# Performance work log

Hardware: AMD Instinct MI355X
Metric: run time of the kernel (lower is better)

Reference implementation:

```python
import jax, jax.numpy as jnp
import numpy as np

B, S, T = 32, 64, 64          # batch, src_len, tgt_len
E, H, V = 512, 1024, 32000    # embed, hidden, vocab
WSCALE = 0.05                 # keep tanh/sigmoid in sane range


def setup_inputs() -> dict:
    key = jax.random.key(0)
    ks = jax.random.split(key, 14)
    n = lambda k, shp: jax.random.normal(k, shp, jnp.float32)
    return {
        "target": jax.random.randint(ks[0], (B, T), 0, V),
        "src_enc": n(ks[1], (B, S, 2 * H)),
        "h0": n(ks[2], (B, H)),
        "c0": n(ks[3], (B, H)),
        "emb": n(ks[4], (V, E)) * WSCALE,
        "W_ih": n(ks[5], (E, 4 * H)) * WSCALE,
        "W_hh": n(ks[6], (H, 4 * H)) * WSCALE,
        "b_rnn": jnp.zeros((4 * H,), jnp.float32),
        "W_attn": n(ks[7], (2 * H, H)) * WSCALE,
        "b_attn": jnp.zeros((H,), jnp.float32),
        "W_comb": n(ks[8], (2 * H, H)) * WSCALE,
        "b_comb": jnp.zeros((H,), jnp.float32),
        "W_out": n(ks[9], (H, V)) * WSCALE,
        "b_out": jnp.zeros((V,), jnp.float32),
    }


def reference(target, src_enc, h0, c0, emb, W_ih, W_hh, b_rnn,
              W_attn, b_attn, W_comb, b_comb, W_out, b_out):
    # Pre-project encoder states once (decode() applies attention.linear up front)
    enc_proj = src_enc @ W_attn + b_attn                 # [B,S,H]
    xs = emb[target[:, :-1]]                             # teacher forcing [B,T-1,E]
    xs = jnp.swapaxes(xs, 0, 1)                          # [T-1,B,E] for scan

    def step(carry, x_t):
        h, c = carry
        # LSTM cell (torch gate order i, f, g, o)
        gates = x_t @ W_ih + h @ W_hh + b_rnn            # [B,4H]
        i, f, g, o = jnp.split(gates, 4, axis=-1)
        c = jax.nn.sigmoid(f) * c + jax.nn.sigmoid(i) * jnp.tanh(g)
        h = jax.nn.sigmoid(o) * jnp.tanh(c)
        # Bilinear attention: score = h^T (W_attn e_s) over source positions
        scores = jnp.einsum('bsh,bh->bs', enc_proj, h)
        attn = jax.nn.softmax(scores, axis=-1)
        ctx = jnp.einsum('bs,bsh->bh', attn, enc_proj)   # [B,H]
        out = jnp.tanh(jnp.concatenate([h, ctx], axis=-1) @ W_comb + b_comb)
        return (h, c), out

    _, outs = jax.lax.scan(step, (h0, c0), xs)           # [T-1,B,H]
    outs = jnp.swapaxes(outs, 0, 1)                      # [B,T-1,H]
    logits = outs @ W_out + b_out                        # [B,T-1,V]
    return logits
```

## Files before the change

### kernel.cpp

```cpp
#include <hip/hip_runtime.h>
#include <stdint.h>

#define NB    32
#define NS    64
#define TDEC  63
#define NE    512
#define NH    1024
#define NV    32000

typedef float  floatx4 __attribute__((ext_vector_type(4)));
typedef short  short8  __attribute__((ext_vector_type(8)));
typedef short  short4v __attribute__((ext_vector_type(4)));

__device__ __forceinline__ float bf2f(short s) {
  return __uint_as_float(((uint32_t)(uint16_t)s) << 16);
}
__device__ __forceinline__ short f2bf(float f) {
  uint32_t u = __float_as_uint(f);
  uint32_t r = (u + 0x7fffu + ((u >> 16) & 1u)) >> 16;
  return (short)(uint16_t)r;
}
__device__ __forceinline__ float sigm(float x) { return 1.f / (1.f + expf(-x)); }

template<int PERM>
__global__ __launch_bounds__(256) void transpose_bf(
    const float* __restrict__ W, short* __restrict__ Wt, int K, int N)
{
  __shared__ float tile[32][33];
  int k0 = blockIdx.x * 32, n0 = blockIdx.y * 32;
  int tx = threadIdx.x & 31, ty = threadIdx.x >> 5;
#pragma unroll
  for (int r = 0; r < 32; r += 8)
    tile[ty + r][tx] = W[(size_t)(k0 + ty + r) * N + n0 + tx];
  __syncthreads();
  int kq = threadIdx.x & 7, nl = threadIdx.x >> 3;
  int n = n0 + nl;
  int rr = PERM ? ((n & 1023) * 4 + (n >> 10)) : n;
  short4v v;
#pragma unroll
  for (int q = 0; q < 4; ++q) v[q] = f2bf(tile[kq * 4 + q][nl]);
  *(short4v*)&Wt[(size_t)rr * K + k0 + kq * 4] = v;
}

template<int PERM>
__global__ __launch_bounds__(256) void transpose_bf_split(
    const float* __restrict__ W, short* __restrict__ Wt_hi,
    short* __restrict__ Wt_lo, int K, int N)
{
  __shared__ float tile[32][33];
  int k0 = blockIdx.x * 32, n0 = blockIdx.y * 32;
  int tx = threadIdx.x & 31, ty = threadIdx.x >> 5;
#pragma unroll
  for (int r = 0; r < 32; r += 8)
    tile[ty + r][tx] = W[(size_t)(k0 + ty + r) * N + n0 + tx];
  __syncthreads();
  int kq = threadIdx.x & 7, nl = threadIdx.x >> 3;
  int n = n0 + nl;
  int rr = PERM ? ((n & 1023) * 4 + (n >> 10)) : n;
  short4v vh, vl;
#pragma unroll
  for (int q = 0; q < 4; ++q) {
    float v = tile[kq * 4 + q][nl];
    short h = f2bf(v);
    vh[q] = h;
    vl[q] = f2bf(v - bf2f(h));
  }
  size_t o = (size_t)rr * K + k0 + kq * 4;
  *(short4v*)&Wt_hi[o] = vh;
  *(short4v*)&Wt_lo[o] = vl;
}

__global__ __launch_bounds__(256) void gather_init(
    const int* __restrict__ target, const float* __restrict__ emb,
    const float* __restrict__ h0, const float* __restrict__ c0,
    const float* __restrict__ brnn,
    short* __restrict__ xs, float* __restrict__ hf_all,
    short* __restrict__ hhi_all, short* __restrict__ hlo_all,
    float* __restrict__ c_buf, float* __restrict__ brnn_p)
{
  const int NXS = TDEC * NB * NE;
  const int HN = NH * NB;
  int total = NXS + 2 * HN + 4096;
  for (int idx = blockIdx.x * 256 + threadIdx.x; idx < total; idx += gridDim.x * 256) {
    if (idx < NXS) {
      int row = idx >> 9, e = idx & 511;
      int t = row >> 5, b = row & 31;
      int token = target[b * 64 + t];
      xs[idx] = f2bf(emb[(size_t)token * NE + e]);
    } else if (idx < NXS + HN) {
      int r = idx - NXS;
      float v = h0[r];
      hf_all[r] = v;
      short hh = f2bf(v);
      hhi_all[r] = hh;
      hlo_all[r] = f2bf(v - bf2f(hh));
    } else if (idx < NXS + 2 * HN) {
      int r = idx - NXS - HN;
      c_buf[r] = c0[r];
    } else {
      int c = idx - NXS - 2 * HN;
      brnn_p[c] = brnn[(c & 3) * 1024 + (c >> 2)];
    }
  }
}

template<int OUT_BF>
__global__ __launch_bounds__(256) void gemm_kernel(
    const short* __restrict__ Ab, const short* __restrict__ Bt,
    void* __restrict__ Cptr, const float* __restrict__ bias,
    int M, int N, int K)
{
  __shared__ short As[128 * 40];
  __shared__ short Bs[128 * 40];
  __shared__ float cst[OUT_BF ? 1 : 32 * 132];
  const int m0 = blockIdx.x * 128;
  const int n0 = blockIdx.y * 128;
  const int tid = threadIdx.x;
  const int lane = tid & 63;
  const int wid = tid >> 6;
  const int wr = wid >> 1, wc = wid & 1;

  floatx4 acc[4][4] = {};
  const int row = tid >> 1;
  const int kh  = (tid & 1) << 4;

  for (int k0 = 0; k0 < K; k0 += 32) {
    {
      int gm = m0 + row;
      short8 lo, hi;
      if (gm < M) {
        const short* src = Ab + (size_t)gm * K + k0 + kh;
        lo = *(const short8*)src;
        hi = *(const short8*)(src + 8);
      } else {
#pragma unroll
        for (int c = 0; c < 8; ++c) { lo[c] = 0; hi[c] = 0; }
      }
      *(short8*)&As[row * 40 + kh]     = lo;
      *(short8*)&As[row * 40 + kh + 8] = hi;
    }
    {
      const short* src = Bt + (size_t)(n0 + row) * K + k0 + kh;
      *(short8*)&Bs[row * 40 + kh]     = *(const short8*)src;
      *(short8*)&Bs[row * 40 + kh + 8] = *(const short8*)(src + 8);
    }
    __syncthreads();

    const int kA = (lane >> 4) << 3;
    const int rsel = lane & 15;
    short8 af[4], bfr[4];
#pragma unroll
    for (int mi = 0; mi < 4; ++mi)
      af[mi] = *(const short8*)&As[(wr * 64 + mi * 16 + rsel) * 40 + kA];
#pragma unroll
    for (int ni = 0; ni < 4; ++ni)
      bfr[ni] = *(const short8*)&Bs[(wc * 64 + ni * 16 + rsel) * 40 + kA];
#pragma unroll
    for (int mi = 0; mi < 4; ++mi)
#pragma unroll
      for (int ni = 0; ni < 4; ++ni)
        acc[mi][ni] = __builtin_amdgcn_mfma_f32_16x16x32_bf16(af[mi], bfr[ni], acc[mi][ni], 0, 0, 0);
    __syncthreads();
  }

  const int crow = (lane >> 4) * 4;
  const int ccol = lane & 15;
  if (OUT_BF) {
#pragma unroll
    for (int mi = 0; mi < 4; ++mi) {
#pragma unroll
      for (int ni = 0; ni < 4; ++ni) {
        int gn = n0 + wc * 64 + ni * 16 + ccol;
        float bv = bias[gn];
#pragma unroll
        for (int i = 0; i < 4; ++i) {
          int gm = m0 + wr * 64 + mi * 16 + crow + i;
          if (gm < M)
            ((short*)Cptr)[(size_t)gm * N + gn] = f2bf(acc[mi][ni][i] + bv);
        }
      }
    }
  } else {
#pragma unroll
    for (int p = 0; p < 4; ++p) {
      __syncthreads();
      if (wr == (p >> 1)) {
        int mi0 = (p & 1) * 2;
#pragma unroll
        for (int mm = 0; mm < 2; ++mm) {
#pragma unroll
          for (int ni = 0; ni < 4; ++ni) {
            int c = wc * 64 + ni * 16 + ccol;
#pragma unroll
            for (int i = 0; i < 4; ++i)
              cst[(mm * 16 + crow + i) * 132 + c] = acc[mi0 + mm][ni][i];
          }
        }
      }
      __syncthreads();
#pragma unroll
      for (int rep = 0; rep < 4; ++rep) {
        int cell = tid + rep * 256;
        int r = cell >> 5, q = cell & 31;
        int gm = m0 + p * 32 + r;
        int gn = n0 + q * 4;
        if (gm < M) {
          float4 bv = *(const float4*)&bias[gn];
          float4 v;
          v.x = cst[r * 132 + q * 4 + 0] + bv.x;
          v.y = cst[r * 132 + q * 4 + 1] + bv.y;
          v.z = cst[r * 132 + q * 4 + 2] + bv.z;
          v.w = cst[r * 132 + q * 4 + 3] + bv.w;
          *(float4*)&((float*)Cptr)[(size_t)gm * N + gn] = v;
        }
      }
    }
  }
}

__global__ __launch_bounds__(256) void gemm_split(
    const float* __restrict__ A, const short* __restrict__ Bt_hi,
    const short* __restrict__ Bt_lo, float* __restrict__ C,
    const float* __restrict__ bias, int M, int N, int K)
{
  __shared__ short As_hi[128 * 40];
  __shared__ short As_lo[128 * 40];
  __shared__ short Bs_hi[128 * 40];
  __shared__ short Bs_lo[128 * 40];
  const int m0 = blockIdx.x * 128;
  const int n0 = blockIdx.y * 128;
  const int tid = threadIdx.x;
  const int lane = tid & 63;
  const int wid = tid >> 6;
  const int wr = wid >> 1, wc = wid & 1;

  floatx4 acc[4][4] = {};
  const int row = tid >> 1;
  const int kh  = (tid & 1) << 4;

  for (int k0 = 0; k0 < K; k0 += 32) {
    {
      const float* src = A + (size_t)(m0 + row) * K + k0 + kh;
      short8 h0v, h1, l0, l1;
#pragma unroll
      for (int c = 0; c < 8; ++c) {
        float v = src[c];
        short h = f2bf(v); h0v[c] = h; l0[c] = f2bf(v - bf2f(h));
        float w = src[c + 8];
        short g = f2bf(w); h1[c] = g; l1[c] = f2bf(w - bf2f(g));
      }
      *(short8*)&As_hi[row * 40 + kh]     = h0v;
      *(short8*)&As_hi[row * 40 + kh + 8] = h1;
      *(short8*)&As_lo[row * 40 + kh]     = l0;
      *(short8*)&As_lo[row * 40 + kh + 8] = l1;
    }
    {
      size_t o = (size_t)(n0 + row) * K + k0 + kh;
      *(short8*)&Bs_hi[row * 40 + kh]     = *(const short8*)(Bt_hi + o);
      *(short8*)&Bs_hi[row * 40 + kh + 8] = *(const short8*)(Bt_hi + o + 8);
      *(short8*)&Bs_lo[row * 40 + kh]     = *(const short8*)(Bt_lo + o);
      *(short8*)&Bs_lo[row * 40 + kh + 8] = *(const short8*)(Bt_lo + o + 8);
    }
    __syncthreads();

    const int kA = (lane >> 4) << 3;
    const int rsel = lane & 15;
    short8 ah[4], al[4], bh[4], bl[4];
#pragma unroll
    for (int mi = 0; mi < 4; ++mi) {
      int off = (wr * 64 + mi * 16 + rsel) * 40 + kA;
      ah[mi] = *(const short8*)&As_hi[off];
      al[mi] = *(const short8*)&As_lo[off];
    }
#pragma unroll
    for (int ni = 0; ni < 4; ++ni) {
      int off = (wc * 64 + ni * 16 + rsel) * 40 + kA;
      bh[ni] = *(const short8*)&Bs_hi[off];
      bl[ni] = *(const short8*)&Bs_lo[off];
    }
#pragma unroll
    for (int mi = 0; mi < 4; ++mi)
#pragma unroll
      for (int ni = 0; ni < 4; ++ni) {
        floatx4 a = acc[mi][ni];
        a = __builtin_amdgcn_mfma_f32_16x16x32_bf16(al[mi], bh[ni], a, 0, 0, 0);
        a = __builtin_amdgcn_mfma_f32_16x16x32_bf16(ah[mi], bl[ni], a, 0, 0, 0);
        a = __builtin_amdgcn_mfma_f32_16x16x32_bf16(ah[mi], bh[ni], a, 0, 0, 0);
        acc[mi][ni] = a;
      }
    __syncthreads();
  }

  const int crow = (lane >> 4) * 4;
  const int ccol = lane & 15;
#pragma unroll
  for (int mi = 0; mi < 4; ++mi) {
#pragma unroll
    for (int ni = 0; ni < 4; ++ni) {
      int gn = n0 + wc * 64 + ni * 16 + ccol;
      float bv = bias[gn];
#pragma unroll
      for (int i = 0; i < 4; ++i) {
        int gm = m0 + wr * 64 + mi * 16 + crow + i;
        C[(size_t)gm * N + gn] = acc[mi][ni][i] + bv;
      }
    }
  }
}

__global__ __launch_bounds__(512) void scan_a(
    int t,
    const short* __restrict__ Whp_hi,
    const short* __restrict__ Whp_lo,
    const short* __restrict__ gatesx,
    short* __restrict__ hhi_all,
    short* __restrict__ hlo_all,
    float* __restrict__ hf_all,
    float* __restrict__ c_buf)
{
  __shared__ float smem[8 * 32 * 33];
  const int blk = blockIdx.x;
  const int tid = threadIdx.x;
  const int lane = tid & 63;
  const int wid = tid >> 6;
  const int rsel = lane & 15;
  const int kA = (lane >> 4) * 8;
  const int crow = (lane >> 4) * 4;
  const int ccol = lane & 15;

  const size_t spv = (size_t)t * (NH * NB);
  const size_t snw = (size_t)(t + 1) * (NH * NB);
  const short* Hh = hhi_all + spv;
  const short* Hl = hlo_all + spv;
  const int c0 = blk * 32;
  const int kb = wid * 128;

  floatx4 acc[2][2] = {};
  const short* wh0 = Whp_hi + (size_t)(c0 + rsel) * NH + kb + kA;
  const short* wl0 = Whp_lo + (size_t)(c0 + rsel) * NH + kb + kA;
  const short* wh1 = Whp_hi + (size_t)(c0 + 16 + rsel) * NH + kb + kA;
  const short* wl1 = Whp_lo + (size_t)(c0 + 16 + rsel) * NH + kb + kA;
  const short* ha0 = Hh + (size_t)rsel * NH + kb + kA;
  const short* la0 = Hl + (size_t)rsel * NH + kb + kA;
  const short* ha1 = Hh + (size_t)(16 + rsel) * NH + kb + kA;
  const short* la1 = Hl + (size_t)(16 + rsel) * NH + kb + kA;
#pragma unroll
  for (int kk = 0; kk < 4; ++kk) {
    int k0 = kk * 32;
    short8 a0h = *(const short8*)(ha0 + k0);
    short8 a0l = *(const short8*)(la0 + k0);
    short8 a1h = *(const short8*)(ha1 + k0);
    short8 a1l = *(const short8*)(la1 + k0);
    short8 b0h = *(const short8*)(wh0 + k0);
    short8 b0l = *(const short8*)(wl0 + k0);
    short8 b1h = *(const short8*)(wh1 + k0);
    short8 b1l = *(const short8*)(wl1 + k0);
    acc[0][0] = __builtin_amdgcn_mfma_f32_16x16x32_bf16(a0l, b0h, acc[0][0], 0, 0, 0);
    acc[0][0] = __builtin_amdgcn_mfma_f32_16x16x32_bf16(a0h, b0l, acc[0][0], 0, 0, 0);
    acc[0][0] = __builtin_amdgcn_mfma_f32_16x16x32_bf16(a0h, b0h, acc[0][0], 0, 0, 0);
    acc[0][1] = __builtin_amdgcn_mfma_f32_16x16x32_bf16(a0l, b1h, acc[0][1], 0, 0, 0);
    acc[0][1] = __builtin_amdgcn_mfma_f32_16x16x32_bf16(a0h, b1l, acc[0][1], 0, 0, 0);
    acc[0][1] = __builtin_amdgcn_mfma_f32_16x16x32_bf16(a0h, b1h, acc[0][1], 0, 0, 0);
    acc[1][0] = __builtin_amdgcn_mfma_f32_16x16x32_bf16(a1l, b0h, acc[1][0], 0, 0, 0);
    acc[1][0] = __builtin_amdgcn_mfma_f32_16x16x32_bf16(a1h, b0l, acc[1][0], 0, 0, 0);
    acc[1][0] = __builtin_amdgcn_mfma_f32_16x16x32_bf16(a1h, b0h, acc[1][0], 0, 0, 0);
    acc[1][1] = __builtin_amdgcn_mfma_f32_16x16x32_bf16(a1l, b1h, acc[1][1], 0, 0, 0);
    acc[1][1] = __builtin_amdgcn_mfma_f32_16x16x32_bf16(a1h, b1l, acc[1][1], 0, 0, 0);
    acc[1][1] = __builtin_amdgcn_mfma_f32_16x16x32_bf16(a1h, b1h, acc[1][1], 0, 0, 0);
  }
#pragma unroll
  for (int mi = 0; mi < 2; ++mi)
#pragma unroll
    for (int ni = 0; ni < 2; ++ni)
#pragma unroll
      for (int i = 0; i < 4; ++i)
        smem[wid * 1056 + (mi * 16 + crow + i) * 33 + ni * 16 + ccol] = acc[mi][ni][i];
  __syncthreads();
  if (tid < 256) {
    int b = tid & 31, jl = tid >> 5;
    float g[4];
#pragma unroll
    for (int q = 0; q < 4; ++q) {
      float s = 0;
#pragma unroll
      for (int w = 0; w < 8; ++w) s += smem[w * 1056 + b * 33 + jl * 4 + q];
      g[q] = s;
    }
    int jg = (c0 >> 2) + jl;
    const short* gx = gatesx + ((size_t)t * 32 + b) * 4096 + c0 + jl * 4;
    short4v gxv = *(const short4v*)gx;
    float gi = g[0] + bf2f(gxv[0]);
    float gf = g[1] + bf2f(gxv[1]);
    float gg = g[2] + bf2f(gxv[2]);
    float go = g[3] + bf2f(gxv[3]);
    float co = c_buf[b * NH + jg];
    float cn = sigm(gf) * co + sigm(gi) * tanhf(gg);
    float hn = sigm(go) * tanhf(cn);
    c_buf[b * NH + jg] = cn;
    hf_all[snw + b * NH + jg] = hn;
    short hh = f2bf(hn);
    hhi_all[snw + b * NH + jg] = hh;
    hlo_all[snw + b * NH + jg] = f2bf(hn - bf2f(hh));
  }
}

__global__ __launch_bounds__(256) void attn_batch(
    const float* __restrict__ encp,
    const float* __restrict__ hf_all,
    short* __restrict__ ctxhi_all,
    short* __restrict__ ctxlo_all)
{
  __shared__ float h_lds[NH];
  __shared__ float part[4 * 64];
  __shared__ float sc_lds[64];
  __shared__ float p_lds[64];
  const int blk = blockIdx.x;
  const int b = blk / TDEC;
  const int t = blk % TDEC;
  const int tid = threadIdx.x;
  const float* h = hf_all + ((size_t)(t + 1) * 32 + b) * NH;

  ((float4*)h_lds)[tid] = ((const float4*)h)[tid];
  __syncthreads();
  {
    int s = tid & 63, kc = tid >> 6;
    const float4* ep = (const float4*)(encp + ((size_t)(b * 64 + s)) * NH + kc * 256);
    const float4* hp = (const float4*)(h_lds + kc * 256);
    float ac0 = 0, ac1 = 0, ac2 = 0, ac3 = 0;
#pragma unroll
    for (int i = 0; i < 64; i += 4) {
      float4 e0 = ep[i],     h0v = hp[i];
      float4 e1 = ep[i + 1], h1v = hp[i + 1];
      float4 e2 = ep[i + 2], h2v = hp[i + 2];
      float4 e3 = ep[i + 3], h3v = hp[i + 3];
      ac0 = fmaf(e0.x, h0v.x, ac0); ac0 = fmaf(e0.y, h0v.y, ac0);
      ac0 = fmaf(e0.z, h0v.z, ac0); ac0 = fmaf(e0.w, h0v.w, ac0);
      ac1 = fmaf(e1.x, h1v.x, ac1); ac1 = fmaf(e1.y, h1v.y, ac1);
      ac1 = fmaf(e1.z, h1v.z, ac1); ac1 = fmaf(e1.w, h1v.w, ac1);
      ac2 = fmaf(e2.x, h2v.x, ac2); ac2 = fmaf(e2.y, h2v.y, ac2);
      ac2 = fmaf(e2.z, h2v.z, ac2); ac2 = fmaf(e2.w, h2v.w, ac2);
      ac3 = fmaf(e3.x, h3v.x, ac3); ac3 = fmaf(e3.y, h3v.y, ac3);
      ac3 = fmaf(e3.z, h3v.z, ac3); ac3 = fmaf(e3.w, h3v.w, ac3);
    }
    part[kc * 64 + s] = (ac0 + ac1) + (ac2 + ac3);
  }
  __syncthreads();
  if (tid < 64) {
    float sc = part[tid] + part[64 + tid] + part[128 + tid] + part[192 + tid];
    sc_lds[tid] = sc;
    float m = sc;
#pragma unroll
    for (int off = 32; off; off >>= 1) m = fmaxf(m, __shfl_xor(m, off));
    float e = expf(sc - m);
    float sum = e;
#pragma unroll
    for (int off = 32; off; off >>= 1) sum += __shfl_xor(sum, off);
    p_lds[tid] = e / sum;
  }
  __syncthreads();
  {
    int k4 = tid * 4;
    float a0 = 0, a1 = 0, a2 = 0, a3 = 0;
    const float* ep = encp + (size_t)(b * 64) * NH + k4;
    for (int s = 0; s < 64; ++s) {
      float p = p_lds[s];
      float4 e = *(const float4*)(ep + (size_t)s * NH);
      a0 = fmaf(p, e.x, a0); a1 = fmaf(p, e.y, a1);
      a2 = fmaf(p, e.z, a2); a3 = fmaf(p, e.w, a3);
    }
    size_t crow = ((size_t)t * 32 + b) * NH + k4;
    short4v c4h, c4l;
    float av[4] = {a0, a1, a2, a3};
#pragma unroll
    for (int q = 0; q < 4; ++q) {
      short hh = f2bf(av[q]);
      c4h[q] = hh;
      c4l[q] = f2bf(av[q] - bf2f(hh));
    }
    *(short4v*)(ctxhi_all + crow) = c4h;
    *(short4v*)(ctxlo_all + crow) = c4l;
  }
}

__global__ __launch_bounds__(256) void gemm_comb(
    const short* __restrict__ Ah_hi,
    const short* __restrict__ Ah_lo,
    const short* __restrict__ Cx_hi,
    const short* __restrict__ Cx_lo,
    const short* __restrict__ Bt_hi,
    const short* __restrict__ Bt_lo,
    const float* __restrict__ bcomb,
    short* __restrict__ outs)
{
  __shared__ short As_hi[128 * 40];
  __shared__ short As_lo[128 * 40];
  __shared__ short Bs_hi[128 * 40];
  __shared__ short Bs_lo[128 * 40];
  const int m0 = blockIdx.x * 128;
  const int n0 = blockIdx.y * 128;
  const int tid = threadIdx.x;
  const int lane = tid & 63;
  const int wid = tid >> 6;
  const int wr = wid >> 1, wc = wid & 1;

  floatx4 acc[4][4] = {};
  const int row = tid >> 1;
  const int kh  = (tid & 1) << 4;

  for (int k0 = 0; k0 < 2048; k0 += 32) {
    {
      int gr = m0 + row;
      const short* sh;
      const short* sl;
      if (k0 < NH) {
        sh = Ah_hi + (size_t)gr * NH + k0 + kh;
        sl = Ah_lo + (size_t)gr * NH + k0 + kh;
      } else {
        sh = Cx_hi + (size_t)gr * NH + (k0 - NH) + kh;
        sl = Cx_lo + (size_t)gr * NH + (k0 - NH) + kh;
      }
      *(short8*)&As_hi[row * 40 + kh]     = *(const short8*)sh;
      *(short8*)&As_hi[row * 40 + kh + 8] = *(const short8*)(sh + 8);
      *(short8*)&As_lo[row * 40 + kh]     = *(const short8*)sl;
      *(short8*)&As_lo[row * 40 + kh + 8] = *(const short8*)(sl + 8);
    }
    {
      size_t o = (size_t)(n0 + row) * 2048 + k0 + kh;
      *(short8*)&Bs_hi[row * 40 + kh]     = *(const short8*)(Bt_hi + o);
      *(short8*)&Bs_hi[row * 40 + kh + 8] = *(const short8*)(Bt_hi + o + 8);
      *(short8*)&Bs_lo[row * 40 + kh]     = *(const short8*)(Bt_lo + o);
      *(short8*)&Bs_lo[row * 40 + kh + 8] = *(const short8*)(Bt_lo + o + 8);
    }
    __syncthreads();

    const int kA = (lane >> 4) << 3;
    const int rsel = lane & 15;
    short8 ah[4], al[4], bh[4], bl[4];
#pragma unroll
    for (int mi = 0; mi < 4; ++mi) {
      int off = (wr * 64 + mi * 16 + rsel) * 40 + kA;
      ah[mi] = *(const short8*)&As_hi[off];
      al[mi] = *(const short8*)&As_lo[off];
    }
#pragma unroll
    for (int ni = 0; ni < 4; ++ni) {
      int off = (wc * 64 + ni * 16 + rsel) * 40 + kA;
      bh[ni] = *(const short8*)&Bs_hi[off];
      bl[ni] = *(const short8*)&Bs_lo[off];
    }
#pragma unroll
    for (int mi = 0; mi < 4; ++mi)
#pragma unroll
      for (int ni = 0; ni < 4; ++ni) {
        floatx4 a = acc[mi][ni];
        a = __builtin_amdgcn_mfma_f32_16x16x32_bf16(al[mi], bh[ni], a, 0, 0, 0);
        a = __builtin_amdgcn_mfma_f32_16x16x32_bf16(ah[mi], bl[ni], a, 0, 0, 0);
        a = __builtin_amdgcn_mfma_f32_16x16x32_bf16(ah[mi], bh[ni], a, 0, 0, 0);
        acc[mi][ni] = a;
      }
    __syncthreads();
  }

  const int crow = (lane >> 4) * 4;
  const int ccol = lane & 15;
#pragma unroll
  for (int mi = 0; mi < 4; ++mi) {
#pragma unroll
    for (int ni = 0; ni < 4; ++ni) {
      int gn = n0 + wc * 64 + ni * 16 + ccol;
      float bv = bcomb[gn];
#pragma unroll
      for (int i = 0; i < 4; ++i) {
        int gm = m0 + wr * 64 + mi * 16 + crow + i;
        if (gm < TDEC * NB) {
          int tt = gm >> 5, bb = gm & 31;
          outs[((size_t)bb * TDEC + tt) * NH + gn] = f2bf(tanhf(acc[mi][ni][i] + bv));
        }
      }
    }
  }
}

extern "C" void kernel_launch(void* const* d_in, const int* in_sizes, int n_in,
                              void* d_out, int out_size, void* d_ws, size_t ws_size,
                              hipStream_t stream)
{
  const int*   target = (const int*)  d_in[0];
  const float* src    = (const float*)d_in[1];
  const float* h0     = (const float*)d_in[2];
  const float* c0     = (const float*)d_in[3];
  const float* emb    = (const float*)d_in[4];
  const float* Wih    = (const float*)d_in[5];
  const float* Whh    = (const float*)d_in[6];
  const float* brnn   = (const float*)d_in[7];
  const float* Wattn  = (const float*)d_in[8];
  const float* battn  = (const float*)d_in[9];
  const float* Wcomb  = (const float*)d_in[10];
  const float* bcomb  = (const float*)d_in[11];
  const float* Wout   = (const float*)d_in[12];
  const float* bout   = (const float*)d_in[13];
  float* out = (float*)d_out;

  char* ws = (char*)d_ws;
  size_t off = 0;
  auto take = [&](size_t bytes) { char* p = ws + off; off += (bytes + 255) & ~(size_t)255; return p; };
  short* WoutT    = (short*)take((size_t)NV * NH * 2);
  short* WattnTh  = (short*)take((size_t)NH * 2048 * 2);
  short* WattnTl  = (short*)take((size_t)NH * 2048 * 2);
  short* WihTp    = (short*)take((size_t)4096 * NE * 2);
  short* WhpHi    = (short*)take((size_t)4096 * NH * 2);
  short* WhpLo    = (short*)take((size_t)4096 * NH * 2);
  short* WcTHi    = (short*)take((size_t)NH * 2048 * 2);
  short* WcTLo    = (short*)take((size_t)NH * 2048 * 2);
  short* xs_bf    = (short*)take((size_t)TDEC * NB * NE * 2);
  float* encp     = (float*)take((size_t)NB * NS * NH * 4);
  short* gatesx   = (short*)take((size_t)TDEC * NB * 4096 * 2);
  short* outs_bf  = (short*)take((size_t)TDEC * NB * NH * 2);
  float* hf_all   = (float*)take((size_t)65 * NB * NH * 4);
  short* hhi_all  = (short*)take((size_t)65 * NB * NH * 2);
  short* hlo_all  = (short*)take((size_t)65 * NB * NH * 2);
  short* ctxhi_a  = (short*)take((size_t)2048 * NH * 2);
  short* ctxlo_a  = (short*)take((size_t)2048 * NH * 2);
  float* c_buf    = (float*)take((size_t)NH * NB * 4);
  float* brnn_p   = (float*)take((size_t)4096 * 4);
  if (off > ws_size) return;

  transpose_bf_split<0><<<dim3(2048 / 32, NH / 32), 256, 0, stream>>>(Wattn, WattnTh, WattnTl, 2048, NH);
  transpose_bf<1><<<dim3(NE / 32, 4096 / 32), 256, 0, stream>>>(Wih, WihTp, NE, 4096);
  transpose_bf_split<1><<<dim3(NH / 32, 4096 / 32), 256, 0, stream>>>(Whh, WhpHi, WhpLo, NH, 4096);
  transpose_bf_split<0><<<dim3(2048 / 32, NH / 32), 256, 0, stream>>>(Wcomb, WcTHi, WcTLo, 2048, NH);
  transpose_bf<0><<<dim3(NH / 32, NV / 32), 256, 0, stream>>>(Wout, WoutT, NH, NV);
  gather_init<<<1024, 256, 0, stream>>>(target, emb, h0, c0, brnn,
                                        xs_bf, hf_all, hhi_all, hlo_all, c_buf, brnn_p);
  gemm_split<<<dim3(16, NH / 128), 256, 0, stream>>>(src, WattnTh, WattnTl, encp, battn, 2048, NH, 2048);
  gemm_kernel<1><<<dim3(16, 4096 / 128), 256, 0, stream>>>(xs_bf, WihTp, gatesx, brnn_p, TDEC * NB, 4096, NE);
  for (int t = 0; t < TDEC; ++t)
    scan_a<<<128, 512, 0, stream>>>(t, WhpHi, WhpLo, gatesx, hhi_all, hlo_all, hf_all, c_buf);
  attn_batch<<<TDEC * NB, 256, 0, stream>>>(encp, hf_all, ctxhi_a, ctxlo_a);
  gemm_comb<<<dim3(16, 8), 256, 0, stream>>>(hhi_all + (size_t)32 * NH, hlo_all + (size_t)32 * NH,
                                             ctxhi_a, ctxlo_a, WcTHi, WcTLo, bcomb, outs_bf);
  gemm_kernel<0><<<dim3(16, NV / 128), 256, 0, stream>>>(outs_bf, WoutT, out, bout, TDEC * NB, NV, NH);
}
```

Measured before the change: 1.282 ms.

## Fuse LSTM recurrence into one persistent cooperative kernel with grid sync

Replaces the 63 per-timestep scan_a launches with a single cooperative kernel that loops over time and uses grid.sync() between steps. The cell state c now lives in a register instead of a global buffer, and the c0 copy is dropped from gather_init. This removes per-step launch overhead and the c_buf round trips through memory. In exchange it relies on cooperative launch support and pays for a grid-wide barrier on every step.

Result: slower. 1.976 ms (+54.2%).

```diff
diff --git a/kernel.cpp b/kernel.cpp
--- a/kernel.cpp
+++ b/kernel.cpp
@@ -1,4 +1,5 @@
 #include <hip/hip_runtime.h>
+#include <hip/hip_cooperative_groups.h>
 #include <stdint.h>
 
 #define NB    32
@@ -72,15 +73,14 @@
 
 __global__ __launch_bounds__(256) void gather_init(
     const int* __restrict__ target, const float* __restrict__ emb,
-    const float* __restrict__ h0, const float* __restrict__ c0,
-    const float* __restrict__ brnn,
+    const float* __restrict__ h0, const float* __restrict__ brnn,
     short* __restrict__ xs, float* __restrict__ hf_all,
     short* __restrict__ hhi_all, short* __restrict__ hlo_all,
-    float* __restrict__ c_buf, float* __restrict__ brnn_p)
+    float* __restrict__ brnn_p)
 {
   const int NXS = TDEC * NB * NE;
   const int HN = NH * NB;
-  int total = NXS + 2 * HN + 4096;
+  int total = NXS + HN + 4096;
   for (int idx = blockIdx.x * 256 + threadIdx.x; idx < total; idx += gridDim.x * 256) {
     if (idx < NXS) {
       int row = idx >> 9, e = idx & 511;
@@ -94,11 +94,8 @@
       short hh = f2bf(v);
       hhi_all[r] = hh;
       hlo_all[r] = f2bf(v - bf2f(hh));
-    } else if (idx < NXS + 2 * HN) {
-      int r = idx - NXS - HN;
-      c_buf[r] = c0[r];
     } else {
-      int c = idx - NXS - 2 * HN;
+      int c = idx - NXS - HN;
       brnn_p[c] = brnn[(c & 3) * 1024 + (c >> 2)];
     }
   }
@@ -308,16 +305,16 @@
   }
 }
 
-__global__ __launch_bounds__(512) void scan_a(
-    int t,
+__global__ __launch_bounds__(512) void scan_coop(
     const short* __restrict__ Whp_hi,
     const short* __restrict__ Whp_lo,
     const short* __restrict__ gatesx,
     short* __restrict__ hhi_all,
     short* __restrict__ hlo_all,
     float* __restrict__ hf_all,
-    float* __restrict__ c_buf)
-{
+    const float* __restrict__ c0_in)
+{
+  cooperative_groups::grid_group grid = cooperative_groups::this_grid();
   __shared__ float smem[8 * 32 * 33];
   const int blk = blockIdx.x;
   const int tid = threadIdx.x;
@@ -327,80 +324,84 @@
   const int kA = (lane >> 4) * 8;
   const int crow = (lane >> 4) * 4;
   const int ccol = lane & 15;
-
-  const size_t spv = (size_t)t * (NH * NB);
-  const size_t snw = (size_t)(t + 1) * (NH * NB);
-  const short* Hh = hhi_all + spv;
-  const short* Hl = hlo_all + spv;
   const int c0 = blk * 32;
   const int kb = wid * 128;
 
-  floatx4 acc[2][2] = {};
   const short* wh0 = Whp_hi + (size_t)(c0 + rsel) * NH + kb + kA;
   const short* wl0 = Whp_lo + (size_t)(c0 + rsel) * NH + kb + kA;
   const short* wh1 = Whp_hi + (size_t)(c0 + 16 + rsel) * NH + kb + kA;
   const short* wl1 = Whp_lo + (size_t)(c0 + 16 + rsel) * NH + kb + kA;
-  const short* ha0 = Hh + (size_t)rsel * NH + kb + kA;
-  const short* la0 = Hl + (size_t)rsel * NH + kb + kA;
-  const short* ha1 = Hh + (size_t)(16 + rsel) * NH + kb + kA;
-  const short* la1 = Hl + (size_t)(16 + rsel) * NH + kb + kA;
-#pragma unroll
-  for (int kk = 0; kk < 4; ++kk) {
-    int k0 = kk * 32;
-    short8 a0h = *(const short8*)(ha0 + k0);
-    short8 a0l = *(const short8*)(la0 + k0);
-    short8 a1h = *(const short8*)(ha1 + k0);
-    short8 a1l = *(const short8*)(la1 + k0);
-    short8 b0h = *(const short8*)(wh0 + k0);
-    short8 b0l = *(const short8*)(wl0 + k0);
-    short8 b1h = *(const short8*)(wh1 + k0);
-    short8 b1l = *(const short8*)(wl1 + k0);
-    acc[0][0] = __builtin_amdgcn_mfma_f32_16x16x32_bf16(a0l, b0h, acc[0][0], 0, 0, 0);
-    acc[0][0] = __builtin_amdgcn_mfma_f32_16x16x32_bf16(a0h, b0l, acc[0][0], 0, 0, 0);
-    acc[0][0] = __builtin_amdgcn_mfma_f32_16x16x32_bf16(a0h, b0h, acc[0][0], 0, 0, 0);
-    acc[0][1] = __builtin_amdgcn_mfma_f32_16x16x32_bf16(a0l, b1h, acc[0][1], 0, 0, 0);
-    acc[0][1] = __builtin_amdgcn_mfma_f32_16x16x32_bf16(a0h, b1l, acc[0][1], 0, 0, 0);
-    acc[0][1] = __builtin_amdgcn_mfma_f32_16x16x32_bf16(a0h, b1h, acc[0][1], 0, 0, 0);
-    acc[1][0] = __builtin_amdgcn_mfma_f32_16x16x32_bf16(a1l, b0h, acc[1][0], 0, 0, 0);
-    acc[1][0] = __builtin_amdgcn_mfma_f32_16x16x32_bf16(a1h, b0l, acc[1][0], 0, 0, 0);
-    acc[1][0] = __builtin_amdgcn_mfma_f32_16x16x32_bf16(a1h, b0h, acc[1][0], 0, 0, 0);
-    acc[1][1] = __builtin_amdgcn_mfma_f32_16x16x32_bf16(a1l, b1h, acc[1][1], 0, 0, 0);
-    acc[1][1] = __builtin_amdgcn_mfma_f32_16x16x32_bf16(a1h, b1l, acc[1][1], 0, 0, 0);
-    acc[1][1] = __builtin_amdgcn_mfma_f32_16x16x32_bf16(a1h, b1h, acc[1][1], 0, 0, 0);
-  }
-#pragma unroll
-  for (int mi = 0; mi < 2; ++mi)
-#pragma unroll
-    for (int ni = 0; ni < 2; ++ni)
-#pragma unroll
-      for (int i = 0; i < 4; ++i)
-        smem[wid * 1056 + (mi * 16 + crow + i) * 33 + ni * 16 + ccol] = acc[mi][ni][i];
-  __syncthreads();
-  if (tid < 256) {
-    int b = tid & 31, jl = tid >> 5;
-    float g[4];
-#pragma unroll
-    for (int q = 0; q < 4; ++q) {
-      float s = 0;
-#pragma unroll
-      for (int w = 0; w < 8; ++w) s += smem[w * 1056 + b * 33 + jl * 4 + q];
-      g[q] = s;
-    }
-    int jg = (c0 >> 2) + jl;
-    const short* gx = gatesx + ((size_t)t * 32 + b) * 4096 + c0 + jl * 4;
-    short4v gxv = *(const short4v*)gx;
-    float gi = g[0] + bf2f(gxv[0]);
-    float gf = g[1] + bf2f(gxv[1]);
-    float gg = g[2] + bf2f(gxv[2]);
-    float go = g[3] + bf2f(gxv[3]);
-    float co = c_buf[b * NH + jg];
-    float cn = sigm(gf) * co + sigm(gi) * tanhf(gg);
-    float hn = sigm(go) * tanhf(cn);
-    c_buf[b * NH + jg] = cn;
-    hf_all[snw + b * NH + jg] = hn;
-    short hh = f2bf(hn);
-    hhi_all[snw + b * NH + jg] = hh;
-    hlo_all[snw + b * NH + jg] = f2bf(hn - bf2f(hh));
+
+  const int pb  = tid & 31;
+  const int pjl = tid >> 5;
+  const int pjg = (c0 >> 2) + (pjl & 7);
+  float c_reg = (tid < 256) ? c0_in[pb * NH + pjg] : 0.f;
+
+  for (int t = 0; t < TDEC; ++t) {
+    const size_t spv = (size_t)t * (NH * NB);
+    const size_t snw = spv + (NH * NB);
+    const short* ha0 = hhi_all + spv + (size_t)rsel * NH + kb + kA;
+    const short* la0 = hlo_all + spv + (size_t)rsel * NH + kb + kA;
+    const short* ha1 = hhi_all + spv + (size_t)(16 + rsel) * NH + kb + kA;
+    const short* la1 = hlo_all + spv + (size_t)(16 + rsel) * NH + kb + kA;
+
+    floatx4 acc[2][2] = {};
+#pragma unroll
+    for (int kk = 0; kk < 4; ++kk) {
+      int k0 = kk * 32;
+      short8 a0h = *(const short8*)(ha0 + k0);
+      short8 a0l = *(const short8*)(la0 + k0);
+      short8 a1h = *(const short8*)(ha1 + k0);
+      short8 a1l = *(const short8*)(la1 + k0);
+      short8 b0h = *(const short8*)(wh0 + k0);
+      short8 b0l = *(const short8*)(wl0 + k0);
+      short8 b1h = *(const short8*)(wh1 + k0);
+      short8 b1l = *(const short8*)(wl1 + k0);
+      acc[0][0] = __builtin_amdgcn_mfma_f32_16x16x32_bf16(a0l, b0h, acc[0][0], 0, 0, 0);
+      acc[0][0] = __builtin_amdgcn_mfma_f32_16x16x32_bf16(a0h, b0l, acc[0][0], 0, 0, 0);
+      acc[0][0] = __builtin_amdgcn_mfma_f32_16x16x32_bf16(a0h, b0h, acc[0][0], 0, 0, 0);
+      acc[0][1] = __builtin_amdgcn_mfma_f32_16x16x32_bf16(a0l, b1h, acc[0][1], 0, 0, 0);
+      acc[0][1] = __builtin_amdgcn_mfma_f32_16x16x32_bf16(a0h, b1l, acc[0][1], 0, 0, 0);
+      acc[0][1] = __builtin_amdgcn_mfma_f32_16x16x32_bf16(a0h, b1h, acc[0][1], 0, 0, 0);
+      acc[1][0] = __builtin_amdgcn_mfma_f32_16x16x32_bf16(a1l, b0h, acc[1][0], 0, 0, 0);
+      acc[1][0] = __builtin_amdgcn_mfma_f32_16x16x32_bf16(a1h, b0l, acc[1][0], 0, 0, 0);
+      acc[1][0] = __builtin_amdgcn_mfma_f32_16x16x32_bf16(a1h, b0h, acc[1][0], 0, 0, 0);
+      acc[1][1] = __builtin_amdgcn_mfma_f32_16x16x32_bf16(a1l, b1h, acc[1][1], 0, 0, 0);
+      acc[1][1] = __builtin_amdgcn_mfma_f32_16x16x32_bf16(a1h, b1l, acc[1][1], 0, 0, 0);
+      acc[1][1] = __builtin_amdgcn_mfma_f32_16x16x32_bf16(a1h, b1h, acc[1][1], 0, 0, 0);
+    }
+#pragma unroll
+    for (int mi = 0; mi < 2; ++mi)
+#pragma unroll
+      for (int ni = 0; ni < 2; ++ni)
+#pragma unroll
+        for (int i = 0; i < 4; ++i)
+          smem[wid * 1056 + (mi * 16 + crow + i) * 33 + ni * 16 + ccol] = acc[mi][ni][i];
+    __syncthreads();
+    if (tid < 256) {
+      float g[4];
+#pragma unroll
+      for (int q = 0; q < 4; ++q) {
+        float s = 0;
+#pragma unroll
+        for (int w = 0; w < 8; ++w) s += smem[w * 1056 + pb * 33 + pjl * 4 + q];
+        g[q] = s;
+      }
+      const short* gx = gatesx + ((size_t)t * 32 + pb) * 4096 + c0 + pjl * 4;
+      short4v gxv = *(const short4v*)gx;
+      float gi = g[0] + bf2f(gxv[0]);
+      float gf = g[1] + bf2f(gxv[1]);
+      float gg = g[2] + bf2f(gxv[2]);
+      float go = g[3] + bf2f(gxv[3]);
+      float cn = sigm(gf) * c_reg + sigm(gi) * tanhf(gg);
+      float hn = sigm(go) * tanhf(cn);
+      c_reg = cn;
+      hf_all[snw + pb * NH + pjg] = hn;
+      short hh = f2bf(hn);
+      hhi_all[snw + pb * NH + pjg] = hh;
+      hlo_all[snw + pb * NH + pjg] = f2bf(hn - bf2f(hh));
+    }
+    grid.sync();
   }
 }
 
@@ -621,7 +622,6 @@
   short* hlo_all  = (short*)take((size_t)65 * NB * NH * 2);
   short* ctxhi_a  = (short*)take((size_t)2048 * NH * 2);
   short* ctxlo_a  = (short*)take((size_t)2048 * NH * 2);
-  float* c_buf    = (float*)take((size_t)NH * NB * 4);
   float* brnn_p   = (float*)take((size_t)4096 * 4);
   if (off > ws_size) return;
 
@@ -630,12 +630,18 @@
   transpose_bf_split<1><<<dim3(NH / 32, 4096 / 32), 256, 0, stream>>>(Whh, WhpHi, WhpLo, NH, 4096);
   transpose_bf_split<0><<<dim3(2048 / 32, NH / 32), 256, 0, stream>>>(Wcomb, WcTHi, WcTLo, 2048, NH);
   transpose_bf<0><<<dim3(NH / 32, NV / 32), 256, 0, stream>>>(Wout, WoutT, NH, NV);
-  gather_init<<<1024, 256, 0, stream>>>(target, emb, h0, c0, brnn,
-                                        xs_bf, hf_all, hhi_all, hlo_all, c_buf, brnn_p);
+  gather_init<<<1024, 256, 0, stream>>>(target, emb, h0, brnn,
+                                        xs_bf, hf_all, hhi_all, hlo_all, brnn_p);
   gemm_split<<<dim3(16, NH / 128), 256, 0, stream>>>(src, WattnTh, WattnTl, encp, battn, 2048, NH, 2048);
   gemm_kernel<1><<<dim3(16, 4096 / 128), 256, 0, stream>>>(xs_bf, WihTp, gatesx, brnn_p, TDEC * NB, 4096, NE);
-  for (int t = 0; t < TDEC; ++t)
-    scan_a<<<128, 512, 0, stream>>>(t, WhpHi, WhpLo, gatesx, hhi_all, hlo_all, hf_all, c_buf);
+  {
+    const short* a0 = WhpHi; const short* a1 = WhpLo; const short* a2 = gatesx;
+    short* a3 = hhi_all; short* a4 = hlo_all; float* a5 = hf_all;
+    const float* a6 = c0;
+    void* kargs[] = {(void*)&a0, (void*)&a1, (void*)&a2, (void*)&a3,
+                     (void*)&a4, (void*)&a5, (void*)&a6};
+    hipLaunchCooperativeKernel((void*)scan_coop, dim3(128), dim3(512), kargs, 0, stream);
+  }
   attn_batch<<<TDEC * NB, 256, 0, stream>>>(encp, hf_all, ctxhi_a, ctxlo_a);
   gemm_comb<<<dim3(16, 8), 256, 0, stream>>>(hhi_all + (size_t)32 * NH, hlo_all + (size_t)32 * NH,
                                              ctxhi_a, ctxlo_a, WcTHi, WcTLo, bcomb, outs_bf);
```
